# Performance work log

Measured on AMD Instinct MI355X. Metric: run time of the kernel, lower is better.

The kernel has to match this reference:

```python
import jax, jax.numpy as jnp
import numpy as np

B, NGT, G, C = 2, 64, 6, 64
NVOX = 100000            # occupied voxels per batch element
STRIDE = 4               # x_conv3 stride
RADIUS = 0.4             # pool radius (meters)
PCR = (0.0, -40.0, -3.0)
VOX = (0.05, 0.05, 0.1)
DZ, DY, DX = 10, 400, 352  # downsampled sparse grid (z, y, x)


def setup_inputs() -> dict:
    key = jax.random.key(0)
    k = jax.random.split(key, 10)
    cx = jax.random.uniform(k[0], (B, NGT, 1), minval=5.0, maxval=65.0)
    cy = jax.random.uniform(k[1], (B, NGT, 1), minval=-35.0, maxval=35.0)
    cz = jax.random.uniform(k[2], (B, NGT, 1), minval=-1.5, maxval=0.5)
    dims = jax.random.uniform(k[3], (B, NGT, 3), minval=1.5, maxval=4.5)
    heading = jax.random.uniform(k[4], (B, NGT, 1), minval=-np.pi, maxval=np.pi)
    label = jax.random.randint(k[5], (B, NGT, 1), 1, 4).astype(jnp.float32)
    gt_boxes = jnp.concatenate([cx, cy, cz, dims, heading, label], -1)

    def make_voxels(kc, kf):
        kz, ky, kx = jax.random.split(kc, 3)
        z = jax.random.randint(kz, (B * NVOX,), 0, DZ)
        y = jax.random.randint(ky, (B * NVOX,), 0, DY)
        x = jax.random.randint(kx, (B * NVOX,), 0, DX)
        b = jnp.repeat(jnp.arange(B), NVOX)
        coords = jnp.stack([b, z, y, x], 1).astype(jnp.int32)  # (N, 4) bzyx
        feats = jax.random.normal(kf, (B * NVOX, C), dtype=jnp.float32)
        return coords, feats

    cd, fd = make_voxels(k[6], k[7])
    cs, fs = make_voxels(k[8], k[9])
    return {"gt_boxes": gt_boxes,
            "voxel_coords_dir": cd, "voxel_feats_dir": fd,
            "voxel_coords_dsr": cs, "voxel_feats_dsr": fs}


def _grid_points(gt_boxes):
    # get_dense_grid_points + rotate_points_along_z + global shift
    rois = gt_boxes.reshape(-1, gt_boxes.shape[-1])  # (R, 8)
    g = jnp.arange(G, dtype=jnp.float32)
    idx = jnp.stack(jnp.meshgrid(g, g, g, indexing='ij'), -1).reshape(-1, 3)  # (G^3, 3)
    size = rois[:, 3:6]
    local = (idx[None] + 0.5) / G * size[:, None] - size[:, None] * 0.5  # (R, G^3, 3)
    h = rois[:, 6]
    c, s = jnp.cos(h)[:, None], jnp.sin(h)[:, None]
    x, y, z = local[..., 0], local[..., 1], local[..., 2]
    rot = jnp.stack([x * c - y * s, x * s + y * c, z], -1)
    return rot + rois[:, None, 0:3]  # (R, G^3, 3) global grid points


def _pool(grid_xyz, grid_zyx, gbatch, coords, feats):
    # voxel2pinds hash table: (B, DZ, DY, DX) -> point index or -1
    Ntot = coords.shape[0]
    v2p = jnp.full((B, DZ, DY, DX), -1, jnp.int32)
    v2p = v2p.at[coords[:, 0], coords[:, 1], coords[:, 2], coords[:, 3]].set(
        jnp.arange(Ntot, dtype=jnp.int32))
    # voxel centers (get_voxel_centers with downsample=STRIDE)
    vsz = jnp.array([VOX[0] * STRIDE, VOX[1] * STRIDE, VOX[2] * STRIDE], jnp.float32)
    vox_xyz = (coords[:, jnp.array([3, 2, 1])].astype(jnp.float32) + 0.5) * vsz + jnp.array(PCR, jnp.float32)
    # 3x3x3 neighbor window (QUERY_RANGES = [1,1,1])
    o = jnp.arange(-1, 2)
    offs = jnp.stack(jnp.meshgrid(o, o, o, indexing='ij'), -1).reshape(-1, 3)  # (27, 3) zyx
    nb = grid_zyx[:, None, :] + offs[None]  # (M, 27, 3)
    dims = jnp.array([DZ, DY, DX])
    inb = jnp.all((nb >= 0) & (nb < dims), -1)
    nbc = jnp.clip(nb, 0, dims - 1)
    flat = ((gbatch[:, None] * DZ + nbc[..., 0]) * DY + nbc[..., 1]) * DX + nbc[..., 2]
    pidx = v2p.reshape(-1)[flat]  # (M, 27)
    valid = inb & (pidx >= 0)
    psafe = jnp.where(valid, pidx, 0)
    nxyz = vox_xyz[psafe]  # (M, 27, 3)
    d2 = jnp.sum((nxyz - grid_xyz[:, None]) ** 2, -1)
    m = (valid & (d2 < RADIUS * RADIUS)).astype(feats.dtype)  # ball-query mask
    nf = feats[psafe]  # (M, 27, C) irregular gather
    return jnp.einsum('mkc,mk->mc', nf, m) / jnp.maximum(m.sum(-1), 1.0)[:, None]


def _forward(gt_boxes, voxel_coords_dir, voxel_feats_dir, voxel_coords_dsr, voxel_feats_dsr):
    grid = _grid_points(gt_boxes)            # (R, G^3, 3)
    grid_xyz = grid.reshape(-1, 3)           # (M, 3)
    cf = jnp.floor((grid_xyz - jnp.array(PCR, jnp.float32)) / jnp.array(VOX, jnp.float32))
    cds = jnp.floor(cf / STRIDE).astype(jnp.int32)  # xyz coords at stride
    grid_zyx = cds[:, ::-1]
    R = gt_boxes.shape[0] * gt_boxes.shape[1]
    gbatch = jnp.repeat(jnp.arange(B), NGT * G ** 3)

    def branch(coords, feats):
        p = _pool(grid_xyz, grid_zyx, gbatch, coords, feats)  # (M, C)
        gfeat = p.reshape(R, G ** 3, C).mean(1)               # avg_pool1d over grid pts
        n = jnp.sqrt(jnp.sum(gfeat ** 2, -1, keepdims=True))
        return gfeat / jnp.maximum(n, 1e-12)                  # F.normalize(dim=1)

    fdir = branch(voxel_coords_dir, voxel_feats_dir)
    fdsr = branch(voxel_coords_dsr, voxel_feats_dsr)
    return jnp.mean(jnp.abs(jnp.sum(fdir * fdsr, -1)))


def reference(gt_boxes, voxel_coords_dir, voxel_feats_dir, voxel_coords_dsr, voxel_feats_dsr):
    return _forward(gt_boxes, voxel_coords_dir, voxel_feats_dir, voxel_coords_dsr, voxel_feats_dsr)
```

## Files before the change

kernel.cpp:

```cpp
#include <hip/hip_runtime.h>

#define B_     2
#define NGT_   64
#define G_     6
#define C_     64
#define NVOX_  100000
#define DZ_    10
#define DY_    400
#define DX_    352
#define NPTS   (B_ * NVOX_)
#define NROI   (B_ * NGT_)
#define NGP    (G_ * G_ * G_)
#define M_     (NROI * NGP)
#define VCELLS (B_ * DZ_ * DY_ * DX_)

#define WPB    8
#define JPR    (NGP / WPB)
#define SCAT_BLOCKS ((2 * NPTS + 255) / 256)
#define POOL_BLOCKS (2 * M_ / WPB)

__global__ __launch_bounds__(256) void scatter_kernel(
    const int* __restrict__ cdir, const int* __restrict__ cdsr,
    int* __restrict__ v2p, float* __restrict__ out) {
  int i = blockIdx.x * 256 + threadIdx.x;
  if (i == 0) out[0] = 0.0f;
  if (i >= 2 * NPTS) return;
  int br = (i >= NPTS) ? 1 : 0;
  int p  = i - br * NPTS;
  const int* cb = br ? cdsr : cdir;
  int4 v = ((const int4*)cb)[p];
  int flat = ((v.x * DZ_ + v.y) * DY_ + v.z) * DX_ + v.w;
  atomicMax(&v2p[(long long)br * VCELLS + flat], p);
}

__global__ __launch_bounds__(512) void pool_kernel(
    const float* __restrict__ gt,
    const float* __restrict__ fdir, const float* __restrict__ fdsr,
    const int* __restrict__ v2p, float* __restrict__ part) {
#pragma clang fp contract(off)
  __shared__ float red[WPB][C_];
  int wid  = threadIdx.x >> 6;
  int lane = threadIdx.x & 63;
  int w    = blockIdx.x * WPB + wid;
  int br   = (w >= M_) ? 1 : 0;
  int rem  = w - br * M_;
  int roi  = rem / NGP;
  int gp   = rem - roi * NGP;

  const float* fb  = br ? fdsr : fdir;
  const int*   vpb = v2p + (long long)br * VCELLS;

  const float* r8 = gt + roi * 8;
  float cx = r8[0], cy = r8[1], cz = r8[2];
  float d0 = r8[3], d1 = r8[4], d2s = r8[5];
  float h  = r8[6];

  int ii = gp / 36, jj = (gp / 6) % 6, kk = gp % 6;
  float tx = (ii + 0.5f) / 6.0f;
  float ty = (jj + 0.5f) / 6.0f;
  float tz = (kk + 0.5f) / 6.0f;
  float lx = tx * d0 - d0 * 0.5f;
  float ly = ty * d1 - d1 * 0.5f;
  float lz = tz * d2s - d2s * 0.5f;
  float ch = cosf(h), sh = sinf(h);
  float gx = (lx * ch - ly * sh) + cx;
  float gy = (lx * sh + ly * ch) + cy;
  float gz = lz + cz;

  float fx = floorf((gx - 0.0f)   / 0.05f);
  float fy = floorf((gy + 40.0f)  / 0.05f);
  float fz = floorf((gz + 3.0f)   / 0.1f);
  int ixc = (int)floorf(fx * 0.25f);
  int iyc = (int)floorf(fy * 0.25f);
  int izc = (int)floorf(fz * 0.25f);

  int b = roi >> 6;

  int  pidx_l = -1;
  bool valid  = false;
  if (lane < 27) {
    int oz = lane / 9 - 1, oy = (lane / 3) % 3 - 1, ox = lane % 3 - 1;
    int nz = izc + oz, ny = iyc + oy, nx = ixc + ox;
    if (nz >= 0 && nz < DZ_ && ny >= 0 && ny < DY_ && nx >= 0 && nx < DX_) {
      float vx = ((float)nx + 0.5f) * 0.2f + 0.0f;
      float vy = ((float)ny + 0.5f) * 0.2f + (-40.0f);
      float vz = ((float)nz + 0.5f) * 0.4f + (-3.0f);
      float ddx = vx - gx, ddy = vy - gy, ddz = vz - gz;
      float dd = (ddx * ddx + ddy * ddy) + ddz * ddz;
      if (dd < 0.16f) {
        int flat = ((b * DZ_ + nz) * DY_ + ny) * DX_ + nx;
        int p = vpb[flat];
        if (p >= 0) { valid = true; pidx_l = p; }
      }
    }
  }

  unsigned long long ball = __ballot(valid);
  int cnt = __popcll(ball);
  float acc = 0.0f;
  unsigned long long mm = ball;
  while (mm) {
    int p0, p1 = -1, p2 = -1, p3 = -1;
    { int k = (int)__builtin_ctzll(mm); mm &= mm - 1; p0 = __shfl(pidx_l, k, 64); }
    if (mm) { int k = (int)__builtin_ctzll(mm); mm &= mm - 1; p1 = __shfl(pidx_l, k, 64); }
    if (mm) { int k = (int)__builtin_ctzll(mm); mm &= mm - 1; p2 = __shfl(pidx_l, k, 64); }
    if (mm) { int k = (int)__builtin_ctzll(mm); mm &= mm - 1; p3 = __shfl(pidx_l, k, 64); }
    float v0 = fb[(long long)p0 * C_ + lane];
    float v1 = (p1 >= 0) ? fb[(long long)p1 * C_ + lane] : 0.0f;
    float v2 = (p2 >= 0) ? fb[(long long)p2 * C_ + lane] : 0.0f;
    float v3 = (p3 >= 0) ? fb[(long long)p3 * C_ + lane] : 0.0f;
    acc += v0;
    if (p1 >= 0) acc += v1;
    if (p2 >= 0) acc += v2;
    if (p3 >= 0) acc += v3;
  }
  float pooled = acc / fmaxf((float)cnt, 1.0f);

  red[wid][lane] = pooled;
  __syncthreads();
  if (wid == 0) {
    float s = 0.0f;
#pragma unroll
    for (int q = 0; q < WPB; ++q) s += red[q][lane];
    part[(long long)blockIdx.x * C_ + lane] = s;
  }
}

__global__ __launch_bounds__(64) void reduce_final_kernel(
    const float* __restrict__ part, float* __restrict__ out) {
  int t = threadIdx.x;
  int r = blockIdx.x;
  const float* pa = part + (long long)r * JPR * C_;
  const float* pb = part + (long long)(NROI * JPR + r * JPR) * C_;
  float a = 0.0f, b = 0.0f;
#pragma unroll
  for (int j = 0; j < JPR; ++j) a += pa[j * C_ + t];
#pragma unroll
  for (int j = 0; j < JPR; ++j) b += pb[j * C_ + t];
  float dot = a * b, na = a * a, nb = b * b;
  for (int off = 32; off; off >>= 1) {
    dot += __shfl_xor(dot, off, 64);
    na  += __shfl_xor(na,  off, 64);
    nb  += __shfl_xor(nb,  off, 64);
  }
  if (t == 0) {
    float term = fabsf(dot) / (fmaxf(sqrtf(na), 1e-12f) * fmaxf(sqrtf(nb), 1e-12f));
    atomicAdd(out, term * (1.0f / 128.0f));
  }
}

extern "C" void kernel_launch(void* const* d_in, const int* in_sizes, int n_in,
                              void* d_out, int out_size, void* d_ws, size_t ws_size,
                              hipStream_t stream) {
  const float* gt   = (const float*)d_in[0];
  const int*   cdir = (const int*)d_in[1];
  const float* fdir = (const float*)d_in[2];
  const int*   cdsr = (const int*)d_in[3];
  const float* fdsr = (const float*)d_in[4];
  float* out = (float*)d_out;

  int*   v2p  = (int*)d_ws;
  float* part = (float*)((char*)d_ws + (size_t)2 * VCELLS * 4);

  scatter_kernel<<<SCAT_BLOCKS, 256, 0, stream>>>(cdir, cdsr, v2p, out);
  pool_kernel<<<POOL_BLOCKS, 512, 0, stream>>>(gt, fdir, fdsr, v2p, part);
  reduce_final_kernel<<<NROI, 64, 0, stream>>>(part, out);
}
```

Before: 160.4 us.

## Process both branches per wave, sharing grid-point geometry and neighbor tests

Each wave now handles one grid point for both the dir and dsr branches, instead of one wave per branch per grid point. The grid-point rotation, voxel-coordinate and 27-neighbor radius tests are computed once and reused for both voxel maps. The gather loop interleaves the feature loads from both tensors to expose more memory-level parallelism. This halves the block count and roughly doubles per-wave work and registers. Partial sums go to two separate output regions that the final reduction reads.

Result: faster. 151.5 us (-5.6%).

```diff
diff --git a/kernel.cpp b/kernel.cpp
--- a/kernel.cpp
+++ b/kernel.cpp
@@ -16,8 +16,9 @@
 
 #define WPB    8
 #define JPR    (NGP / WPB)
+#define PROWS  (M_ / WPB)
 #define SCAT_BLOCKS ((2 * NPTS + 255) / 256)
-#define POOL_BLOCKS (2 * M_ / WPB)
+#define POOL_BLOCKS PROWS
 
 __global__ __launch_bounds__(256) void scatter_kernel(
     const int* __restrict__ cdir, const int* __restrict__ cdsr,
@@ -38,17 +39,12 @@
     const float* __restrict__ fdir, const float* __restrict__ fdsr,
     const int* __restrict__ v2p, float* __restrict__ part) {
 #pragma clang fp contract(off)
-  __shared__ float red[WPB][C_];
+  __shared__ float red[2][WPB][C_];
   int wid  = threadIdx.x >> 6;
   int lane = threadIdx.x & 63;
-  int w    = blockIdx.x * WPB + wid;
-  int br   = (w >= M_) ? 1 : 0;
-  int rem  = w - br * M_;
-  int roi  = rem / NGP;
-  int gp   = rem - roi * NGP;
-
-  const float* fb  = br ? fdsr : fdir;
-  const int*   vpb = v2p + (long long)br * VCELLS;
+  int roi  = blockIdx.x / JPR;
+  int j    = blockIdx.x - roi * JPR;
+  int gp   = j * WPB + wid;
 
   const float* r8 = gt + roi * 8;
   float cx = r8[0], cy = r8[1], cz = r8[2];
@@ -76,8 +72,8 @@
 
   int b = roi >> 6;
 
-  int  pidx_l = -1;
-  bool valid  = false;
+  bool geo  = false;
+  int  flat = 0;
   if (lane < 27) {
     int oz = lane / 9 - 1, oy = (lane / 3) % 3 - 1, ox = lane % 3 - 1;
     int nz = izc + oz, ny = iyc + oy, nx = ixc + ox;
@@ -88,41 +84,61 @@
       float ddx = vx - gx, ddy = vy - gy, ddz = vz - gz;
       float dd = (ddx * ddx + ddy * ddy) + ddz * ddz;
       if (dd < 0.16f) {
-        int flat = ((b * DZ_ + nz) * DY_ + ny) * DX_ + nx;
-        int p = vpb[flat];
-        if (p >= 0) { valid = true; pidx_l = p; }
+        geo  = true;
+        flat = ((b * DZ_ + nz) * DY_ + ny) * DX_ + nx;
       }
     }
   }
+  int p0 = -1, p1 = -1;
+  if (geo) {
+    p0 = v2p[flat];
+    p1 = v2p[VCELLS + flat];
+  }
 
-  unsigned long long ball = __ballot(valid);
-  int cnt = __popcll(ball);
-  float acc = 0.0f;
-  unsigned long long mm = ball;
-  while (mm) {
-    int p0, p1 = -1, p2 = -1, p3 = -1;
-    { int k = (int)__builtin_ctzll(mm); mm &= mm - 1; p0 = __shfl(pidx_l, k, 64); }
-    if (mm) { int k = (int)__builtin_ctzll(mm); mm &= mm - 1; p1 = __shfl(pidx_l, k, 64); }
-    if (mm) { int k = (int)__builtin_ctzll(mm); mm &= mm - 1; p2 = __shfl(pidx_l, k, 64); }
-    if (mm) { int k = (int)__builtin_ctzll(mm); mm &= mm - 1; p3 = __shfl(pidx_l, k, 64); }
-    float v0 = fb[(long long)p0 * C_ + lane];
-    float v1 = (p1 >= 0) ? fb[(long long)p1 * C_ + lane] : 0.0f;
-    float v2 = (p2 >= 0) ? fb[(long long)p2 * C_ + lane] : 0.0f;
-    float v3 = (p3 >= 0) ? fb[(long long)p3 * C_ + lane] : 0.0f;
-    acc += v0;
-    if (p1 >= 0) acc += v1;
-    if (p2 >= 0) acc += v2;
-    if (p3 >= 0) acc += v3;
+  unsigned long long ball0 = __ballot(geo && p0 >= 0);
+  unsigned long long ball1 = __ballot(geo && p1 >= 0);
+  int cnt0 = __popcll(ball0), cnt1 = __popcll(ball1);
+  float acc0 = 0.0f, acc1 = 0.0f;
+  unsigned long long m0 = ball0, m1 = ball1;
+  while (m0 | m1) {
+    int a0 = -1, a1 = -1, a2 = -1, a3 = -1;
+    int b0 = -1, b1 = -1, b2 = -1, b3 = -1;
+    if (m0) { int k = (int)__builtin_ctzll(m0); m0 &= m0 - 1; a0 = __shfl(p0, k, 64); }
+    if (m0) { int k = (int)__builtin_ctzll(m0); m0 &= m0 - 1; a1 = __shfl(p0, k, 64); }
+    if (m0) { int k = (int)__builtin_ctzll(m0); m0 &= m0 - 1; a2 = __shfl(p0, k, 64); }
+    if (m0) { int k = (int)__builtin_ctzll(m0); m0 &= m0 - 1; a3 = __shfl(p0, k, 64); }
+    if (m1) { int k = (int)__builtin_ctzll(m1); m1 &= m1 - 1; b0 = __shfl(p1, k, 64); }
+    if (m1) { int k = (int)__builtin_ctzll(m1); m1 &= m1 - 1; b1 = __shfl(p1, k, 64); }
+    if (m1) { int k = (int)__builtin_ctzll(m1); m1 &= m1 - 1; b2 = __shfl(p1, k, 64); }
+    if (m1) { int k = (int)__builtin_ctzll(m1); m1 &= m1 - 1; b3 = __shfl(p1, k, 64); }
+    float va0 = (a0 >= 0) ? fdir[(long long)a0 * C_ + lane] : 0.0f;
+    float va1 = (a1 >= 0) ? fdir[(long long)a1 * C_ + lane] : 0.0f;
+    float va2 = (a2 >= 0) ? fdir[(long long)a2 * C_ + lane] : 0.0f;
+    float va3 = (a3 >= 0) ? fdir[(long long)a3 * C_ + lane] : 0.0f;
+    float vb0 = (b0 >= 0) ? fdsr[(long long)b0 * C_ + lane] : 0.0f;
+    float vb1 = (b1 >= 0) ? fdsr[(long long)b1 * C_ + lane] : 0.0f;
+    float vb2 = (b2 >= 0) ? fdsr[(long long)b2 * C_ + lane] : 0.0f;
+    float vb3 = (b3 >= 0) ? fdsr[(long long)b3 * C_ + lane] : 0.0f;
+    if (a0 >= 0) acc0 += va0;
+    if (a1 >= 0) acc0 += va1;
+    if (a2 >= 0) acc0 += va2;
+    if (a3 >= 0) acc0 += va3;
+    if (b0 >= 0) acc1 += vb0;
+    if (b1 >= 0) acc1 += vb1;
+    if (b2 >= 0) acc1 += vb2;
+    if (b3 >= 0) acc1 += vb3;
   }
-  float pooled = acc / fmaxf((float)cnt, 1.0f);
+  float pooled0 = acc0 / fmaxf((float)cnt0, 1.0f);
+  float pooled1 = acc1 / fmaxf((float)cnt1, 1.0f);
 
-  red[wid][lane] = pooled;
+  red[0][wid][lane] = pooled0;
+  red[1][wid][lane] = pooled1;
   __syncthreads();
-  if (wid == 0) {
+  if (wid < 2) {
     float s = 0.0f;
 #pragma unroll
-    for (int q = 0; q < WPB; ++q) s += red[q][lane];
-    part[(long long)blockIdx.x * C_ + lane] = s;
+    for (int q = 0; q < WPB; ++q) s += red[wid][q][lane];
+    part[((long long)wid * PROWS + blockIdx.x) * C_ + lane] = s;
   }
 }
 
@@ -131,7 +147,7 @@
   int t = threadIdx.x;
   int r = blockIdx.x;
   const float* pa = part + (long long)r * JPR * C_;
-  const float* pb = part + (long long)(NROI * JPR + r * JPR) * C_;
+  const float* pb = part + (long long)(PROWS + r * JPR) * C_;
   float a = 0.0f, b = 0.0f;
 #pragma unroll
   for (int j = 0; j < JPR; ++j) a += pa[j * C_ + t];
```
